# Optimization experiments

Hardware: AMD Instinct MI355X
Metric: run time of the kernel (lower is better)

## Reference

```python
import jax, jax.numpy as jnp
import numpy as np


def setup_inputs() -> dict:
    key = jax.random.key(0)
    k1, k2, k3, k4, k5, k6 = jax.random.split(key, 6)
    B, T, U, D, V = 4, 512, 128, 512, 512
    speech = jax.random.normal(k1, (B, T, D), dtype=jnp.float32)
    text = jax.random.normal(k2, (B, U, D), dtype=jnp.float32)
    W = jax.random.normal(k3, (V, D), dtype=jnp.float32) / np.sqrt(D)
    b = jax.random.normal(k4, (V,), dtype=jnp.float32) * 0.01
    speech_len = jax.random.randint(k5, (B,), 1, T + 1, dtype=jnp.int32)
    text_len = jax.random.randint(k6, (B,), 1, U + 1, dtype=jnp.int32)
    return {"speech": speech, "text": text, "W": W, "b": b,
            "speech_len": speech_len, "text_len": text_len}


def reference(speech, text, W, b, speech_len, text_len):
    # RNN-T joint network: broadcast-add encoder and predictor outputs,
    # then project to vocab. speech: [B,T,D], text: [B,U,D].
    joint = speech[:, :, None, :] + text[:, None, :, :]       # [B,T,U,D]
    logits = jnp.einsum('btud,vd->btuv', joint, W) + b         # [B,T,U,V]
    return logits, speech_len, text_len
```

## Files before the change

kernel.cpp:

```cpp
#include <hip/hip_runtime.h>

#define B_ 4
#define T_ 512
#define U_ 128
#define D_ 512
#define V_ 512
#define MS (B_ * T_)
#define MT (B_ * U_)
#define MTOT (MS + MT)
#define LOGITS_ELEMS ((size_t)B_ * T_ * U_ * V_)

#define TM 128
#define TN 64
#define TK 32
#define XSTR 132
#define WSTR 68

#define S_ELEMS ((size_t)MS * V_)
#define TX_ELEMS ((size_t)MT * V_)
#define PSTRIDE (S_ELEMS + TX_ELEMS)
#define PS4 (PSTRIDE / 4)

#define V4_ (V_ / 4)

typedef float f32x4 __attribute__((ext_vector_type(4)));

__global__ __launch_bounds__(256, 2) void gemm_joint(
    const float* __restrict__ speech, const float* __restrict__ text,
    const float* __restrict__ W, const float* __restrict__ bias,
    float* __restrict__ S, float* __restrict__ Tx, int ktiles)
{
    __shared__ float Xt[TK][XSTR];
    __shared__ float Wt[TK][WSTR];

    const int tid = threadIdx.x;
    const int m0 = blockIdx.x * TM;
    const int n0 = blockIdx.y * TN;
    const int z  = blockIdx.z;
    const int kbase = z * ktiles * TK;
    const int tx = tid & 15;
    const int ty = tid >> 4;

    S  += (size_t)z * PSTRIDE;
    Tx += (size_t)z * PSTRIDE;

    const float* xbase = (m0 < MS) ? (speech + (size_t)m0 * D_)
                                   : (text + (size_t)(m0 - MS) * D_);

    float acc[8][4] = {};
    float4 xr[4], wr[2];

    #pragma unroll
    for (int i = 0; i < 4; ++i) {
        const int q = tid + 256 * i;
        xr[i] = *(const float4*)(xbase + (size_t)(q >> 3) * D_ + kbase + ((q & 7) << 2));
    }
    #pragma unroll
    for (int i = 0; i < 2; ++i) {
        const int q = tid + 256 * i;
        wr[i] = *(const float4*)(W + (size_t)(n0 + (q >> 3)) * D_ + kbase + ((q & 7) << 2));
    }
    #pragma unroll
    for (int i = 0; i < 4; ++i) {
        const int q = tid + 256 * i;
        const int r = q >> 3, c = (q & 7) << 2;
        Xt[c + 0][r] = xr[i].x; Xt[c + 1][r] = xr[i].y;
        Xt[c + 2][r] = xr[i].z; Xt[c + 3][r] = xr[i].w;
    }
    #pragma unroll
    for (int i = 0; i < 2; ++i) {
        const int q = tid + 256 * i;
        const int r = q >> 3, c = (q & 7) << 2;
        Wt[c + 0][r] = wr[i].x; Wt[c + 1][r] = wr[i].y;
        Wt[c + 2][r] = wr[i].z; Wt[c + 3][r] = wr[i].w;
    }
    __syncthreads();

    for (int t = 0; t < ktiles; ++t) {
        if (t + 1 < ktiles) {
            const int kn = kbase + (t + 1) * TK;
            #pragma unroll
            for (int i = 0; i < 4; ++i) {
                const int q = tid + 256 * i;
                xr[i] = *(const float4*)(xbase + (size_t)(q >> 3) * D_ + kn + ((q & 7) << 2));
            }
            #pragma unroll
            for (int i = 0; i < 2; ++i) {
                const int q = tid + 256 * i;
                wr[i] = *(const float4*)(W + (size_t)(n0 + (q >> 3)) * D_ + kn + ((q & 7) << 2));
            }
        }

        #pragma unroll 8
        for (int k = 0; k < TK; ++k) {
            const float4 a0 = *(const float4*)&Xt[k][ty * 8];
            const float4 a1 = *(const float4*)&Xt[k][ty * 8 + 4];
            const float4 b0 = *(const float4*)&Wt[k][tx * 4];
            const float av[8] = {a0.x, a0.y, a0.z, a0.w, a1.x, a1.y, a1.z, a1.w};
            const float bv[4] = {b0.x, b0.y, b0.z, b0.w};
            #pragma unroll
            for (int i = 0; i < 8; ++i)
                #pragma unroll
                for (int j = 0; j < 4; ++j)
                    acc[i][j] += av[i] * bv[j];
        }

        if (t + 1 < ktiles) {
            __syncthreads();
            #pragma unroll
            for (int i = 0; i < 4; ++i) {
                const int q = tid + 256 * i;
                const int r = q >> 3, c = (q & 7) << 2;
                Xt[c + 0][r] = xr[i].x; Xt[c + 1][r] = xr[i].y;
                Xt[c + 2][r] = xr[i].z; Xt[c + 3][r] = xr[i].w;
            }
            #pragma unroll
            for (int i = 0; i < 2; ++i) {
                const int q = tid + 256 * i;
                const int r = q >> 3, c = (q & 7) << 2;
                Wt[c + 0][r] = wr[i].x; Wt[c + 1][r] = wr[i].y;
                Wt[c + 2][r] = wr[i].z; Wt[c + 3][r] = wr[i].w;
            }
            __syncthreads();
        }
    }

    const int vbase = n0 + tx * 4;
    #pragma unroll
    for (int i = 0; i < 8; ++i) {
        const int m = m0 + ty * 8 + i;
        float4 o;
        o.x = acc[i][0]; o.y = acc[i][1]; o.z = acc[i][2]; o.w = acc[i][3];
        if (m < MS) {
            *(float4*)(S + (size_t)m * V_ + vbase) = o;
        } else {
            if (kbase == 0) {
                o.x += bias[vbase + 0];
                o.y += bias[vbase + 1];
                o.z += bias[vbase + 2];
                o.w += bias[vbase + 3];
            }
            *(float4*)(Tx + (size_t)(m - MS) * V_ + vbase) = o;
        }
    }
}

template <bool SPLIT>
__global__ __launch_bounds__(256, 8) void bcast_add(
    const float* __restrict__ S, const float* __restrict__ Tx,
    const int* __restrict__ sl, const int* __restrict__ tl,
    float* __restrict__ out)
{
    const int V4 = V4_;
    const int bid = blockIdx.x;
    const int xcd = bid & 7;
    const int b   = xcd >> 1;
    const int t   = ((bid >> 3) << 1) | (xcd & 1);
    const int bt  = (b << 9) | t;
    const int tid = threadIdx.x;

    if (bt == 0 && tid < 2 * B_) {
        out[LOGITS_ELEMS + tid] = (tid < B_) ? (float)sl[tid]
                                             : (float)tl[tid - B_];
    }

    const f32x4* S4 = (const f32x4*)S + (size_t)bt * V4;
    const f32x4* T4 = (const f32x4*)Tx + (size_t)b * U_ * V4;
    f32x4* O4 = (f32x4*)out + (size_t)bt * U_ * V4;

    f32x4 sv = S4[tid & (V4 - 1)];
    if (SPLIT) sv += S4[PS4 + (tid & (V4 - 1))];

    #pragma unroll 8
    for (int idx = tid; idx < U_ * V4; idx += 256) {
        f32x4 tv = T4[idx];
        if (SPLIT) tv += T4[PS4 + idx];
        __builtin_nontemporal_store(sv + tv, &O4[idx]);
    }
}

extern "C" void kernel_launch(void* const* d_in, const int* in_sizes, int n_in,
                              void* d_out, int out_size, void* d_ws, size_t ws_size,
                              hipStream_t stream) {
    const float* speech = (const float*)d_in[0];
    const float* text   = (const float*)d_in[1];
    const float* W      = (const float*)d_in[2];
    const float* bias   = (const float*)d_in[3];
    const int*   sl     = (const int*)d_in[4];
    const int*   tl     = (const int*)d_in[5];
    float* out = (float*)d_out;

    float* S  = (float*)d_ws;
    float* Tx = S + S_ELEMS;

    const bool split = ws_size >= 2 * PSTRIDE * sizeof(float);

    if (split) {
        dim3 g1(MTOT / TM, V_ / TN, 2);
        gemm_joint<<<g1, 256, 0, stream>>>(speech, text, W, bias, S, Tx, (D_ / TK) / 2);
        bcast_add<true><<<MS, 256, 0, stream>>>(S, Tx, sl, tl, out);
    } else {
        dim3 g1(MTOT / TM, V_ / TN, 1);
        gemm_joint<<<g1, 256, 0, stream>>>(speech, text, W, bias, S, Tx, D_ / TK);
        bcast_add<false><<<MS, 256, 0, stream>>>(S, Tx, sl, tl, out);
    }
}
```

Baseline: 584.5 us.

## Split broadcast-add into U quarters staged through shared memory

The broadcast-add kernel now launches four blocks per (b,t) row. Each block handles a 32-row chunk of the text projection: it stages that chunk, plus the speech row, in shared memory, then writes the sums with nontemporal stores. The XCD-aware block-to-(b,t) mapping is dropped in favour of a plain linear mapping, and launch bounds move from 8 to 2 waves per SIMD. The 64KB of shared memory per block limits occupancy and adds a sync and an extra pass before the stores. The kernel is store-bandwidth bound, so the change aims at smaller blocks with better parallelism but risks worse L2 locality for the text rows.

```diff
diff --git a/kernel.cpp b/kernel.cpp
--- a/kernel.cpp
+++ b/kernel.cpp
@@ -22,6 +22,9 @@
 #define PS4 (PSTRIDE / 4)
 
 #define V4_ (V_ / 4)
+
+#define UQ 4
+#define UCHK (U_ / UQ)
 
 typedef float f32x4 __attribute__((ext_vector_type(4)));
 
@@ -146,36 +149,49 @@
 }
 
 template <bool SPLIT>
-__global__ __launch_bounds__(256, 8) void bcast_add(
+__global__ __launch_bounds__(256, 2) void bcast_add(
     const float* __restrict__ S, const float* __restrict__ Tx,
     const int* __restrict__ sl, const int* __restrict__ tl,
     float* __restrict__ out)
 {
-    const int V4 = V4_;
+    __shared__ float txs[UCHK * V_];
+    __shared__ float svs[V_];
+
+    const int tid = threadIdx.x;
     const int bid = blockIdx.x;
-    const int xcd = bid & 7;
-    const int b   = xcd >> 1;
-    const int t   = ((bid >> 3) << 1) | (xcd & 1);
+    const int uq  = bid & (UQ - 1);
+    const int t   = (bid >> 2) & (T_ - 1);
+    const int b   = bid >> 11;
     const int bt  = (b << 9) | t;
-    const int tid = threadIdx.x;
-
-    if (bt == 0 && tid < 2 * B_) {
+
+    if (bid == 0 && tid < 2 * B_) {
         out[LOGITS_ELEMS + tid] = (tid < B_) ? (float)sl[tid]
                                              : (float)tl[tid - B_];
     }
 
-    const f32x4* S4 = (const f32x4*)S + (size_t)bt * V4;
-    const f32x4* T4 = (const f32x4*)Tx + (size_t)b * U_ * V4;
-    f32x4* O4 = (f32x4*)out + (size_t)bt * U_ * V4;
-
-    f32x4 sv = S4[tid & (V4 - 1)];
-    if (SPLIT) sv += S4[PS4 + (tid & (V4 - 1))];
-
-    #pragma unroll 8
-    for (int idx = tid; idx < U_ * V4; idx += 256) {
-        f32x4 tv = T4[idx];
-        if (SPLIT) tv += T4[PS4 + idx];
-        __builtin_nontemporal_store(sv + tv, &O4[idx]);
+    const f32x4* T4 = (const f32x4*)Tx + ((size_t)b * U_ + uq * UCHK) * V4_;
+    f32x4* txs4 = (f32x4*)txs;
+    #pragma unroll
+    for (int j = 0; j < (UCHK * V4_) / 256; ++j) {
+        const int idx = tid + 256 * j;
+        f32x4 v = T4[idx];
+        if (SPLIT) v += T4[PS4 + idx];
+        txs4[idx] = v;
+    }
+    const f32x4* S4 = (const f32x4*)S + (size_t)bt * V4_;
+    if (tid < V4_) {
+        f32x4 v = S4[tid];
+        if (SPLIT) v += S4[PS4 + tid];
+        ((f32x4*)svs)[tid] = v;
+    }
+    __syncthreads();
+
+    f32x4* O4 = (f32x4*)out + ((size_t)bt * U_ + uq * UCHK) * V4_;
+    const f32x4 sv = ((const f32x4*)svs)[tid & (V4_ - 1)];
+    #pragma unroll
+    for (int j = 0; j < (UCHK * V4_) / 256; ++j) {
+        const int idx = tid + 256 * j;
+        __builtin_nontemporal_store(txs4[idx] + sv, &O4[idx]);
     }
 }
 
@@ -194,14 +210,15 @@
     float* Tx = S + S_ELEMS;
 
     const bool split = ws_size >= 2 * PSTRIDE * sizeof(float);
+    const int nblk2 = B_ * T_ * UQ;
 
     if (split) {
         dim3 g1(MTOT / TM, V_ / TN, 2);
         gemm_joint<<<g1, 256, 0, stream>>>(speech, text, W, bias, S, Tx, (D_ / TK) / 2);
-        bcast_add<true><<<MS, 256, 0, stream>>>(S, Tx, sl, tl, out);
+        bcast_add<true><<<nblk2, 256, 0, stream>>>(S, Tx, sl, tl, out);
     } else {
         dim3 g1(MTOT / TM, V_ / TN, 1);
         gemm_joint<<<g1, 256, 0, stream>>>(speech, text, W, bias, S, Tx, D_ / TK);
-        bcast_add<false><<<MS, 256, 0, stream>>>(S, Tx, sl, tl, out);
+        bcast_add<false><<<nblk2, 256, 0, stream>>>(S, Tx, sl, tl, out);
     }
 }
```

Result: faster. 561.0 us (-4.0%).
